# Performance work log

Measured on AMD Instinct MI355X. Metric: run time of the kernel, lower is better.

## Reference

```python
import jax, jax.numpy as jnp
import numpy as np

N, IN_F, H, D = 3072, 512, 8, 64


def setup_inputs() -> dict:
    key = jax.random.key(0)
    k1, k2, k3, k4, k5 = jax.random.split(key, 5)
    x = jax.random.normal(k1, (N, IN_F), dtype=jnp.float32)
    adj = jax.random.randint(k2, (N, N), 0, 2, dtype=jnp.int32)
    # xavier-uniform-like scales
    s_W = (6.0 / (IN_F + H * D)) ** 0.5
    s_a = (6.0 / (H + D)) ** 0.5
    W = jax.random.uniform(k3, (H * D, IN_F), dtype=jnp.float32, minval=-s_W, maxval=s_W)
    a_src = jax.random.uniform(k4, (H, D), dtype=jnp.float32, minval=-s_a, maxval=s_a)
    a_dst = jax.random.uniform(k5, (H, D), dtype=jnp.float32, minval=-s_a, maxval=s_a)
    return {"x": x, "adj": adj, "W": W, "a_src": a_src, "a_dst": a_dst}


def reference(x, adj, W, a_src, a_dst):
    n = x.shape[0]
    Hh, d = a_src.shape
    h = (x @ W.T).reshape(n, Hh, d)                      # [n, H, d]
    e_src = jnp.einsum('nhd,hd->nh', h, a_src)           # [n, H]
    e_dst = jnp.einsum('nhd,hd->nh', h, a_dst)           # [n, H]
    e = e_src[:, None, :] + e_dst[None, :, :]            # [n, n, H], e[i,j]=src_i+dst_j
    e = jax.nn.leaky_relu(e, negative_slope=0.2)
    mask = (adj + jnp.eye(n, dtype=adj.dtype)) > 0       # [n, n]
    e = jnp.where(mask[:, :, None], e, -jnp.inf)
    alpha = jax.nn.softmax(e, axis=1)                    # softmax over j (neighbors)
    # out[i,h,d] = sum_j alpha[i,j,h] * h[j,h,d]  (dropout=0 / eval mode)
    out = jnp.einsum('ijh,jhd->ihd', alpha, h)
    return out.reshape(n, Hh * d)                        # concat=True
```

## Files before the change

kernel.cpp:

```cpp
#include <hip/hip_runtime.h>
#include <hip/hip_bf16.h>

typedef __bf16 bf16x8 __attribute__((ext_vector_type(8)));
typedef _Float16 half8 __attribute__((ext_vector_type(8)));
typedef _Float16 half2v __attribute__((ext_vector_type(2)));
typedef short s16x2 __attribute__((ext_vector_type(2)));
typedef float f32x4 __attribute__((ext_vector_type(4)));
typedef float f32x16 __attribute__((ext_vector_type(16)));

#define NROW 3072
#define NF 512
#define NH 8
#define ND 64

__device__ __forceinline__ unsigned gat_enc_key(float f) {
    unsigned u = __float_as_uint(f);
    return (f < 0.f) ? ~u : (u | 0x80000000u);
}
__device__ __forceinline__ float gat_dec_key(unsigned k) {
    unsigned u = (k & 0x80000000u) ? (k ^ 0x80000000u) : ~k;
    return __uint_as_float(u);
}

__device__ __forceinline__ bf16x8 gat_ld_cvt8(const float* p) {
    float4 f0 = *reinterpret_cast<const float4*>(p);
    float4 f1 = *reinterpret_cast<const float4*>(p + 4);
    bf16x8 o = { (__bf16)f0.x, (__bf16)f0.y, (__bf16)f0.z, (__bf16)f0.w,
                 (__bf16)f1.x, (__bf16)f1.y, (__bf16)f1.z, (__bf16)f1.w };
    return o;
}

__global__ __launch_bounds__(256) void gat_bitpack(const int* __restrict__ adj,
                                                   unsigned long long* __restrict__ bits64) {
    int wave = threadIdx.x >> 6;
    int lane = threadIdx.x & 63;
    int row = blockIdx.x * 4 + wave;
    const int* p = adj + (long)row * NROW + lane;
    int v[48];
#pragma unroll
    for (int s = 0; s < 48; ++s) v[s] = p[s * 64];
    unsigned long long diag = 1ull << (row & 63);
    int dseg = row >> 6;
#pragma unroll
    for (int s = 0; s < 48; ++s) {
        unsigned long long bal = __ballot(v[s] > 0);
        if (s == dseg) bal |= diag;
        if (lane == 0) bits64[(long)row * 48 + s] = bal;
    }
}

__global__ __launch_bounds__(256) void gat_gemm(const float* __restrict__ x,
                                                const float* __restrict__ W,
                                                _Float16* __restrict__ hT,
                                                const float* __restrict__ a_src,
                                                const float* __restrict__ a_dst,
                                                float* __restrict__ e_srcT,
                                                float* __restrict__ e_dstT,
                                                unsigned* __restrict__ maxkey) {
    __shared__ __align__(16) _Float16 smem[10240];
    __shared__ float ered[2][2][2][32];

    int b = blockIdx.x;
    int i0 = (b >> 3) * 64;
    int o0 = (b & 7) * 64;
    int head = b & 7;
    int tid = threadIdx.x;
    int wave = tid >> 6;
    int lane = tid & 63;
    int half = lane >> 5;
    int l31 = lane & 31;
    int wr = wave >> 1;
    int wc = wave & 1;

    __bf16* sA = reinterpret_cast<__bf16*>(smem);
    __bf16* sB = reinterpret_cast<__bf16*>(smem) + 5120;

    int r = tid >> 2;
    int pp = tid & 3;
    const float* gA = x + (i0 + r) * NF + pp * 8;
    const float* gB = W + (o0 + r) * NF + pp * 8;
    int dslot = r * 40 + pp * 8;

    bf16x8 pA0, pB0, pA1, pB1;
    pA0 = gat_ld_cvt8(gA);
    pB0 = gat_ld_cvt8(gB);
    *reinterpret_cast<bf16x8*>(sA + dslot) = pA0;
    *reinterpret_cast<bf16x8*>(sB + dslot) = pB0;
    pA1 = gat_ld_cvt8(gA + 32);
    pB1 = gat_ld_cvt8(gB + 32);
    __syncthreads();

    f32x16 acc = {};
    int arow = (wr * 32 + l31) * 40;
    int brow = (wc * 32 + l31) * 40;

#pragma unroll
    for (int cc = 0; cc < 8; ++cc) {
        int c0 = cc * 2;
        if (c0 + 2 < 16) {
            pA0 = gat_ld_cvt8(gA + (c0 + 2) * 32);
            pB0 = gat_ld_cvt8(gB + (c0 + 2) * 32);
        }
        {
            const __bf16* pa = sA;
            const __bf16* pb = sB;
#pragma unroll
            for (int ks = 0; ks < 2; ++ks) {
                int q = (((ks << 1) | half)) << 3;
                bf16x8 a = *reinterpret_cast<const bf16x8*>(pa + arow + q);
                bf16x8 bb = *reinterpret_cast<const bf16x8*>(pb + brow + q);
                acc = __builtin_amdgcn_mfma_f32_32x32x16_bf16(a, bb, acc, 0, 0, 0);
            }
        }
        *reinterpret_cast<bf16x8*>(sA + 2560 + dslot) = pA1;
        *reinterpret_cast<bf16x8*>(sB + 2560 + dslot) = pB1;
        __syncthreads();

        int c1 = c0 + 1;
        if (c1 + 2 < 16) {
            pA1 = gat_ld_cvt8(gA + (c1 + 2) * 32);
            pB1 = gat_ld_cvt8(gB + (c1 + 2) * 32);
        }
        {
            const __bf16* pa = sA + 2560;
            const __bf16* pb = sB + 2560;
#pragma unroll
            for (int ks = 0; ks < 2; ++ks) {
                int q = (((ks << 1) | half)) << 3;
                bf16x8 a = *reinterpret_cast<const bf16x8*>(pa + arow + q);
                bf16x8 bb = *reinterpret_cast<const bf16x8*>(pb + brow + q);
                acc = __builtin_amdgcn_mfma_f32_32x32x16_bf16(a, bb, acc, 0, 0, 0);
            }
        }
        if (c1 + 1 < 16) {
            *reinterpret_cast<bf16x8*>(sA + dslot) = pA0;
            *reinterpret_cast<bf16x8*>(sB + dslot) = pB0;
        }
        __syncthreads();
    }

    _Float16* tt = smem + wave * 1280;
#pragma unroll
    for (int reg = 0; reg < 16; ++reg) {
        int rowl = (reg & 3) + 8 * (reg >> 2) + 4 * half;
        tt[rowl * 40 + l31] = (_Float16)acc[reg];
    }
    int orow = lane >> 1;
    int li = (lane & 1) * 16;
    half8 h0, h1;
#pragma unroll
    for (int t = 0; t < 8; ++t) h0[t] = tt[(li + t) * 40 + orow];
#pragma unroll
    for (int t = 0; t < 8; ++t) h1[t] = tt[(li + 8 + t) * 40 + orow];
    _Float16* op = hT + (long)(o0 + wc * 32 + orow) * NROW + i0 + wr * 32 + li;
    *reinterpret_cast<half8*>(op) = h0;
    *reinterpret_cast<half8*>(op + 8) = h1;

    half8 hv0 = *reinterpret_cast<const half8*>(tt + l31 * 40 + half * 16);
    half8 hv1 = *reinterpret_cast<const half8*>(tt + l31 * 40 + half * 16 + 8);
    const float* ap = a_src + head * ND + wc * 32 + half * 16;
    const float* dp = a_dst + head * ND + wc * 32 + half * 16;
    float4 as0 = *reinterpret_cast<const float4*>(ap);
    float4 as1 = *reinterpret_cast<const float4*>(ap + 4);
    float4 as2 = *reinterpret_cast<const float4*>(ap + 8);
    float4 as3 = *reinterpret_cast<const float4*>(ap + 12);
    float4 ad0 = *reinterpret_cast<const float4*>(dp);
    float4 ad1 = *reinterpret_cast<const float4*>(dp + 4);
    float4 ad2 = *reinterpret_cast<const float4*>(dp + 8);
    float4 ad3 = *reinterpret_cast<const float4*>(dp + 12);
    float ps = 0.f, pd = 0.f;
    ps += (float)hv0[0]*as0.x + (float)hv0[1]*as0.y + (float)hv0[2]*as0.z + (float)hv0[3]*as0.w;
    ps += (float)hv0[4]*as1.x + (float)hv0[5]*as1.y + (float)hv0[6]*as1.z + (float)hv0[7]*as1.w;
    ps += (float)hv1[0]*as2.x + (float)hv1[1]*as2.y + (float)hv1[2]*as2.z + (float)hv1[3]*as2.w;
    ps += (float)hv1[4]*as3.x + (float)hv1[5]*as3.y + (float)hv1[6]*as3.z + (float)hv1[7]*as3.w;
    pd += (float)hv0[0]*ad0.x + (float)hv0[1]*ad0.y + (float)hv0[2]*ad0.z + (float)hv0[3]*ad0.w;
    pd += (float)hv0[4]*ad1.x + (float)hv0[5]*ad1.y + (float)hv0[6]*ad1.z + (float)hv0[7]*ad1.w;
    pd += (float)hv1[0]*ad2.x + (float)hv1[1]*ad2.y + (float)hv1[2]*ad2.z + (float)hv1[3]*ad2.w;
    pd += (float)hv1[4]*ad3.x + (float)hv1[5]*ad3.y + (float)hv1[6]*ad3.z + (float)hv1[7]*ad3.w;
    ps += __shfl_xor(ps, 32, 64);
    pd += __shfl_xor(pd, 32, 64);
    if (half == 0) { ered[0][wr][wc][l31] = ps; ered[1][wr][wc][l31] = pd; }
    __syncthreads();
    if (wc == 0) {
        float pst = ered[0][wr][0][l31] + ered[0][wr][1][l31];
        float pdt = ered[1][wr][0][l31] + ered[1][wr][1][l31];
        if (half == 0) {
            e_srcT[head * NROW + i0 + wr * 32 + l31] = pst;
            e_dstT[head * NROW + i0 + wr * 32 + l31] = pdt;
        }
        float mx = pdt;
#pragma unroll
        for (int off = 1; off < 32; off <<= 1) mx = fmaxf(mx, __shfl_xor(mx, off, 64));
        if (lane == 0) atomicMax(&maxkey[head], gat_enc_key(mx));
    }
}

__global__ __launch_bounds__(256) void gat_attn(const unsigned* __restrict__ bits,
                                                const float* __restrict__ e_srcT,
                                                const float* __restrict__ e_dstT,
                                                const unsigned* __restrict__ maxkey,
                                                const _Float16* __restrict__ hT,
                                                _Float16* __restrict__ num,
                                                float* __restrict__ den) {
    constexpr int JCHUNK = NROW / 4;
    constexpr int NC = JCHUNK / 64;
    __shared__ unsigned lds_P[JCHUNK / 2];
    __shared__ unsigned lds_Q[JCHUNK / 2];
    __shared__ __align__(16) _Float16 hbuf[2][4096];
    int b = blockIdx.x;
    int head = b & 7;
    int jc = (b >> 3) & 3;
    int i0 = ((b >> 3) >> 2) * 128;
    int jbase = jc * JCHUNK;
    int tid = threadIdx.x;
    int wave = tid >> 6;
    int lane = tid & 63;
    int half = lane >> 5;
    int l31 = lane & 31;

    float Mg = gat_dec_key(maxkey[head]);
    for (int p = tid; p < JCHUNK / 2; p += 256) {
        float t0 = e_dstT[head * NROW + jbase + 2 * p] - Mg;
        float t1 = e_dstT[head * NROW + jbase + 2 * p + 1] - Mg;
        half2v P = { (_Float16)__expf(t0), (_Float16)__expf(t1) };
        half2v Q = { (_Float16)__expf(0.2f * t0), (_Float16)__expf(0.2f * t1) };
        lds_P[p] = __builtin_bit_cast(unsigned, P);
        lds_Q[p] = __builtin_bit_cast(unsigned, Q);
    }

    int irow = i0 + wave * 32 + l31;
    float u = e_srcT[head * NROW + irow] + Mg;
    float Rf = fminf(__expf(-0.8f * u), 60000.f);
    _Float16 Rh = (_Float16)Rf;
    half2v R2 = { Rh, Rh };
    const half8 ones8 = { (_Float16)1.f, (_Float16)1.f, (_Float16)1.f, (_Float16)1.f,
                          (_Float16)1.f, (_Float16)1.f, (_Float16)1.f, (_Float16)1.f };
    const unsigned* brow = bits + irow * 96 + jc * (JCHUNK / 32);

    int s0 = tid, s1 = tid + 256;
    const _Float16* gp0 = hT + (head * ND + ((s0 >> 6) & 1) * 32 + (s0 & 31)) * NROW
                             + jbase + (s0 >> 7) * 16 + ((s0 >> 5) & 1) * 8;
    const _Float16* gp1 = hT + (head * ND + ((s1 >> 6) & 1) * 32 + (s1 & 31)) * NROW
                             + jbase + (s1 >> 7) * 16 + ((s1 >> 5) & 1) * 8;
    *reinterpret_cast<half8*>(&hbuf[0][tid * 8])         = *reinterpret_cast<const half8*>(gp0);
    *reinterpret_cast<half8*>(&hbuf[0][(tid + 256) * 8]) = *reinterpret_cast<const half8*>(gp1);
    __syncthreads();

    f32x16 acc0 = {};
    f32x16 acc1 = {};
    f32x16 acc2 = {};
    uint2 wm = *reinterpret_cast<const uint2*>(brow);

    for (int k = 0; k < NC; ++k) {
        half8 st0, st1;
        uint2 wmn = wm;
        bool more = (k + 1 < NC);
        if (more) {
            st0 = *reinterpret_cast<const half8*>(gp0 + (k + 1) * 64);
            st1 = *reinterpret_cast<const half8*>(gp1 + (k + 1) * 64);
            wmn = *reinterpret_cast<const uint2*>(brow + (k + 1) * 2);
        }
        const _Float16* hb = &hbuf[k & 1][0];
#pragma unroll
        for (int js = 0; js < 4; ++js) {
            unsigned word = (js < 2) ? wm.x : wm.y;
            unsigned w8 = (word >> ((js & 1) * 16 + half * 8)) & 0xffu;
            unsigned long long S64 = ((unsigned long long)(w8 & 0x55u) << 15)
                                   | ((unsigned long long)(w8 & 0xAAu) << 30);
            uint4 Pv = *reinterpret_cast<const uint4*>(&lds_P[k * 32 + js * 8 + half * 4]);
            uint4 Qv = *reinterpret_cast<const uint4*>(&lds_Q[k * 32 + js * 8 + half * 4]);
            unsigned pr[4] = { Pv.x, Pv.y, Pv.z, Pv.w };
            unsigned qr[4] = { Qv.x, Qv.y, Qv.z, Qv.w };
            unsigned am[4];
#pragma unroll
            for (int t = 0; t < 4; ++t) {
                half2v qq = __builtin_bit_cast(half2v, qr[t]) * R2;
                half2v mx = __builtin_elementwise_max(
                                __builtin_bit_cast(half2v, pr[t]), qq);
                unsigned Wt = (unsigned)(S64 >> (2 * t));
                s16x2 mks = __builtin_bit_cast(s16x2, Wt) >> 15;
                am[t] = __builtin_bit_cast(unsigned, mx)
                      & __builtin_bit_cast(unsigned, mks);
            }
            uint4 m4 = { am[0], am[1], am[2], am[3] };
            half8 af = __builtin_bit_cast(half8, m4);
            half8 v0 = *reinterpret_cast<const half8*>(hb + (js * 128 + lane) * 8);
            half8 v1 = *reinterpret_cast<const half8*>(hb + (js * 128 + 64 + lane) * 8);
            acc0 = __builtin_amdgcn_mfma_f32_32x32x16_f16(af, v0, acc0, 0, 0, 0);
            acc1 = __builtin_amdgcn_mfma_f32_32x32x16_f16(af, v1, acc1, 0, 0, 0);
            acc2 = __builtin_amdgcn_mfma_f32_32x32x16_f16(af, ones8, acc2, 0, 0, 0);
        }
        if (more) {
            *reinterpret_cast<half8*>(&hbuf[(k + 1) & 1][tid * 8])         = st0;
            *reinterpret_cast<half8*>(&hbuf[(k + 1) & 1][(tid + 256) * 8]) = st1;
        }
        wm = wmn;
        __syncthreads();
    }

#pragma unroll
    for (int reg = 0; reg < 16; ++reg) {
        int rowl = (reg & 3) + 8 * (reg >> 2) + 4 * half;
        if (l31 == 0)
            den[(long)(jc * NROW + i0 + wave * 32 + rowl) * NH + head] = acc2[reg];
        long ob = (long)(jc * NROW + i0 + wave * 32 + rowl) * NF + head * ND + l31;
        num[ob]      = (_Float16)acc0[reg];
        num[ob + 32] = (_Float16)acc1[reg];
    }
}

__global__ __launch_bounds__(256) void gat_final(const _Float16* __restrict__ num,
                                                 const float* __restrict__ den,
                                                 float* __restrict__ out) {
    int idx = (blockIdx.x * 256 + threadIdx.x) * 8;
    int i = idx >> 9;
    int c = idx & 511;
    int head = c >> 6;
    half8 n0 = *reinterpret_cast<const half8*>(num + (long)i * NF + c);
    half8 n1 = *reinterpret_cast<const half8*>(num + (long)(NROW + i) * NF + c);
    half8 n2 = *reinterpret_cast<const half8*>(num + (long)(2 * NROW + i) * NF + c);
    half8 n3 = *reinterpret_cast<const half8*>(num + (long)(3 * NROW + i) * NF + c);
    float ds = den[i * NH + head] + den[(NROW + i) * NH + head]
             + den[(2 * NROW + i) * NH + head] + den[(3 * NROW + i) * NH + head];
    float inv = 1.0f / fmaxf(ds, 1e-30f);
    float r0 = ((float)n0[0] + (float)n1[0] + (float)n2[0] + (float)n3[0]) * inv;
    float r1 = ((float)n0[1] + (float)n1[1] + (float)n2[1] + (float)n3[1]) * inv;
    float r2 = ((float)n0[2] + (float)n1[2] + (float)n2[2] + (float)n3[2]) * inv;
    float r3 = ((float)n0[3] + (float)n1[3] + (float)n2[3] + (float)n3[3]) * inv;
    float r4 = ((float)n0[4] + (float)n1[4] + (float)n2[4] + (float)n3[4]) * inv;
    float r5 = ((float)n0[5] + (float)n1[5] + (float)n2[5] + (float)n3[5]) * inv;
    float r6 = ((float)n0[6] + (float)n1[6] + (float)n2[6] + (float)n3[6]) * inv;
    float r7 = ((float)n0[7] + (float)n1[7] + (float)n2[7] + (float)n3[7]) * inv;
    float4 o0 = { r0, r1, r2, r3 };
    float4 o1 = { r4, r5, r6, r7 };
    *reinterpret_cast<float4*>(out + idx)     = o0;
    *reinterpret_cast<float4*>(out + idx + 4) = o1;
}

extern "C" void kernel_launch(void* const* d_in, const int* in_sizes, int n_in,
                              void* d_out, int out_size, void* d_ws, size_t ws_size,
                              hipStream_t stream) {
    const float* x_raw  = (const float*)d_in[0];
    const int*   adj    = (const int*)d_in[1];
    const float* W_raw  = (const float*)d_in[2];
    const float* as_raw = (const float*)d_in[3];
    const float* ad_raw = (const float*)d_in[4];
    float* out = (float*)d_out;

    char* ws = (char*)d_ws;
    _Float16* hT     = (_Float16*)(ws);
    float*    e_srcT = (float*)(ws + 3145728);
    float*    e_dstT = (float*)(ws + 3244032);
    unsigned* maxkey = (unsigned*)(ws + 3342336);
    unsigned* bits   = (unsigned*)(ws + 3342400);
    _Float16* num    = (_Float16*)(ws + 8192064);
    float*    den    = (float*)(ws + 20774976);

    hipMemsetAsync(maxkey, 0, 64, stream);
    gat_bitpack<<<NROW / 4, 256, 0, stream>>>(adj, (unsigned long long*)bits);
    gat_gemm<<<384, 256, 0, stream>>>(x_raw, W_raw, hT, as_raw, ad_raw,
                                      e_srcT, e_dstT, maxkey);
    gat_attn<<<24 * 4 * 8, 256, 0, stream>>>(bits, e_srcT, e_dstT, maxkey, hT, num, den);
    gat_final<<<NROW * NF / 2048, 256, 0, stream>>>(num, den, out);
}
```

Baseline: 140.6 us.

## Merge bitpack into GEMM launch and double rows per attention block

The adjacency bitpack kernel is merged into the GEMM kernel as extra blocks, so the two independent stages run concurrently in one launch and one launch is removed. The attention kernel now handles 256 rows per block instead of 128, with two sets of accumulators sharing each loaded h tile and P/Q values. This halves hT global/LDS traffic per row and the grid size, but raises register pressure (six 16-float accumulators) and leaves only 384 blocks, which may reduce occupancy.

```diff
diff --git a/kernel.cpp b/kernel.cpp
--- a/kernel.cpp
+++ b/kernel.cpp
@@ -12,6 +12,8 @@
 #define NF 512
 #define NH 8
 #define ND 64
+#define BP_BLOCKS 768
+#define GEMM_BLOCKS 384
 
 __device__ __forceinline__ unsigned gat_enc_key(float f) {
     unsigned u = __float_as_uint(f);
@@ -30,43 +32,44 @@
     return o;
 }
 
-__global__ __launch_bounds__(256) void gat_bitpack(const int* __restrict__ adj,
-                                                   unsigned long long* __restrict__ bits64) {
-    int wave = threadIdx.x >> 6;
-    int lane = threadIdx.x & 63;
-    int row = blockIdx.x * 4 + wave;
-    const int* p = adj + (long)row * NROW + lane;
-    int v[48];
-#pragma unroll
-    for (int s = 0; s < 48; ++s) v[s] = p[s * 64];
-    unsigned long long diag = 1ull << (row & 63);
-    int dseg = row >> 6;
-#pragma unroll
-    for (int s = 0; s < 48; ++s) {
-        unsigned long long bal = __ballot(v[s] > 0);
-        if (s == dseg) bal |= diag;
-        if (lane == 0) bits64[(long)row * 48 + s] = bal;
-    }
-}
-
-__global__ __launch_bounds__(256) void gat_gemm(const float* __restrict__ x,
-                                                const float* __restrict__ W,
-                                                _Float16* __restrict__ hT,
-                                                const float* __restrict__ a_src,
-                                                const float* __restrict__ a_dst,
-                                                float* __restrict__ e_srcT,
-                                                float* __restrict__ e_dstT,
-                                                unsigned* __restrict__ maxkey) {
+__global__ __launch_bounds__(256) void gat_gemm_bp(const float* __restrict__ x,
+                                                   const float* __restrict__ W,
+                                                   _Float16* __restrict__ hT,
+                                                   const int* __restrict__ adj,
+                                                   unsigned long long* __restrict__ bits64,
+                                                   const float* __restrict__ a_src,
+                                                   const float* __restrict__ a_dst,
+                                                   float* __restrict__ e_srcT,
+                                                   float* __restrict__ e_dstT,
+                                                   unsigned* __restrict__ maxkey) {
     __shared__ __align__(16) _Float16 smem[10240];
     __shared__ float ered[2][2][2][32];
 
-    int b = blockIdx.x;
+    int tid = threadIdx.x;
+    int wave = tid >> 6;
+    int lane = tid & 63;
+
+    if (blockIdx.x < BP_BLOCKS) {
+        int row = blockIdx.x * 4 + wave;
+        const int* p = adj + (long)row * NROW + lane;
+        int v[48];
+#pragma unroll
+        for (int s = 0; s < 48; ++s) v[s] = p[s * 64];
+        unsigned long long diag = 1ull << (row & 63);
+        int dseg = row >> 6;
+#pragma unroll
+        for (int s = 0; s < 48; ++s) {
+            unsigned long long bal = __ballot(v[s] > 0);
+            if (s == dseg) bal |= diag;
+            if (lane == 0) bits64[(long)row * 48 + s] = bal;
+        }
+        return;
+    }
+
+    int b = blockIdx.x - BP_BLOCKS;
     int i0 = (b >> 3) * 64;
     int o0 = (b & 7) * 64;
     int head = b & 7;
-    int tid = threadIdx.x;
-    int wave = tid >> 6;
-    int lane = tid & 63;
     int half = lane >> 5;
     int l31 = lane & 31;
     int wr = wave >> 1;
@@ -210,7 +213,7 @@
     int b = blockIdx.x;
     int head = b & 7;
     int jc = (b >> 3) & 3;
-    int i0 = ((b >> 3) >> 2) * 128;
+    int i0 = (b >> 5) * 256;
     int jbase = jc * JCHUNK;
     int tid = threadIdx.x;
     int wave = tid >> 6;
@@ -228,14 +231,19 @@
         lds_Q[p] = __builtin_bit_cast(unsigned, Q);
     }
 
-    int irow = i0 + wave * 32 + l31;
-    float u = e_srcT[head * NROW + irow] + Mg;
-    float Rf = fminf(__expf(-0.8f * u), 60000.f);
-    _Float16 Rh = (_Float16)Rf;
-    half2v R2 = { Rh, Rh };
+    int irowA = i0 + wave * 32 + l31;
+    int irowB = irowA + 128;
+    float uA = e_srcT[head * NROW + irowA] + Mg;
+    float uB = e_srcT[head * NROW + irowB] + Mg;
+    float RfA = fminf(__expf(-0.8f * uA), 60000.f);
+    float RfB = fminf(__expf(-0.8f * uB), 60000.f);
+    _Float16 RhA = (_Float16)RfA, RhB = (_Float16)RfB;
+    half2v R2A = { RhA, RhA };
+    half2v R2B = { RhB, RhB };
     const half8 ones8 = { (_Float16)1.f, (_Float16)1.f, (_Float16)1.f, (_Float16)1.f,
                           (_Float16)1.f, (_Float16)1.f, (_Float16)1.f, (_Float16)1.f };
-    const unsigned* brow = bits + irow * 96 + jc * (JCHUNK / 32);
+    const unsigned* browA = bits + (long)irowA * 96 + jc * (JCHUNK / 32);
+    const unsigned* browB = bits + (long)irowB * 96 + jc * (JCHUNK / 32);
 
     int s0 = tid, s1 = tid + 256;
     const _Float16* gp0 = hT + (head * ND + ((s0 >> 6) & 1) * 32 + (s0 & 31)) * NROW
@@ -246,66 +254,84 @@
     *reinterpret_cast<half8*>(&hbuf[0][(tid + 256) * 8]) = *reinterpret_cast<const half8*>(gp1);
     __syncthreads();
 
-    f32x16 acc0 = {};
-    f32x16 acc1 = {};
-    f32x16 acc2 = {};
-    uint2 wm = *reinterpret_cast<const uint2*>(brow);
+    f32x16 acc0a = {}, acc1a = {}, acc2a = {};
+    f32x16 acc0b = {}, acc1b = {}, acc2b = {};
+    uint2 wmA = *reinterpret_cast<const uint2*>(browA);
+    uint2 wmB = *reinterpret_cast<const uint2*>(browB);
 
     for (int k = 0; k < NC; ++k) {
         half8 st0, st1;
-        uint2 wmn = wm;
+        uint2 wmnA = wmA, wmnB = wmB;
         bool more = (k + 1 < NC);
         if (more) {
             st0 = *reinterpret_cast<const half8*>(gp0 + (k + 1) * 64);
             st1 = *reinterpret_cast<const half8*>(gp1 + (k + 1) * 64);
-            wmn = *reinterpret_cast<const uint2*>(brow + (k + 1) * 2);
+            wmnA = *reinterpret_cast<const uint2*>(browA + (k + 1) * 2);
+            wmnB = *reinterpret_cast<const uint2*>(browB + (k + 1) * 2);
         }
         const _Float16* hb = &hbuf[k & 1][0];
 #pragma unroll
         for (int js = 0; js < 4; ++js) {
-            unsigned word = (js < 2) ? wm.x : wm.y;
-            unsigned w8 = (word >> ((js & 1) * 16 + half * 8)) & 0xffu;
-            unsigned long long S64 = ((unsigned long long)(w8 & 0x55u) << 15)
-                                   | ((unsigned long long)(w8 & 0xAAu) << 30);
+            int sh = (js & 1) * 16 + half * 8;
+            unsigned w8A = (((js < 2) ? wmA.x : wmA.y) >> sh) & 0xffu;
+            unsigned w8B = (((js < 2) ? wmB.x : wmB.y) >> sh) & 0xffu;
+            unsigned long long S64A = ((unsigned long long)(w8A & 0x55u) << 15)
+                                    | ((unsigned long long)(w8A & 0xAAu) << 30);
+            unsigned long long S64B = ((unsigned long long)(w8B & 0x55u) << 15)
+                                    | ((unsigned long long)(w8B & 0xAAu) << 30);
             uint4 Pv = *reinterpret_cast<const uint4*>(&lds_P[k * 32 + js * 8 + half * 4]);
             uint4 Qv = *reinterpret_cast<const uint4*>(&lds_Q[k * 32 + js * 8 + half * 4]);
             unsigned pr[4] = { Pv.x, Pv.y, Pv.z, Pv.w };
             unsigned qr[4] = { Qv.x, Qv.y, Qv.z, Qv.w };
-            unsigned am[4];
+            unsigned amA[4], amB[4];
 #pragma unroll
             for (int t = 0; t < 4; ++t) {
-                half2v qq = __builtin_bit_cast(half2v, qr[t]) * R2;
-                half2v mx = __builtin_elementwise_max(
-                                __builtin_bit_cast(half2v, pr[t]), qq);
-                unsigned Wt = (unsigned)(S64 >> (2 * t));
-                s16x2 mks = __builtin_bit_cast(s16x2, Wt) >> 15;
-                am[t] = __builtin_bit_cast(unsigned, mx)
-                      & __builtin_bit_cast(unsigned, mks);
+                half2v pv = __builtin_bit_cast(half2v, pr[t]);
+                half2v qv = __builtin_bit_cast(half2v, qr[t]);
+                half2v mxA = __builtin_elementwise_max(pv, qv * R2A);
+                half2v mxB = __builtin_elementwise_max(pv, qv * R2B);
+                s16x2 mkA = __builtin_bit_cast(s16x2, (unsigned)(S64A >> (2 * t))) >> 15;
+                s16x2 mkB = __builtin_bit_cast(s16x2, (unsigned)(S64B >> (2 * t))) >> 15;
+                amA[t] = __builtin_bit_cast(unsigned, mxA) & __builtin_bit_cast(unsigned, mkA);
+                amB[t] = __builtin_bit_cast(unsigned, mxB) & __builtin_bit_cast(unsigned, mkB);
             }
-            uint4 m4 = { am[0], am[1], am[2], am[3] };
-            half8 af = __builtin_bit_cast(half8, m4);
+            uint4 m4a = { amA[0], amA[1], amA[2], amA[3] };
+            uint4 m4b = { amB[0], amB[1], amB[2], amB[3] };
+            half8 afA = __builtin_bit_cast(half8, m4a);
+            half8 afB = __builtin_bit_cast(half8, m4b);
             half8 v0 = *reinterpret_cast<const half8*>(hb + (js * 128 + lane) * 8);
             half8 v1 = *reinterpret_cast<const half8*>(hb + (js * 128 + 64 + lane) * 8);
-            acc0 = __builtin_amdgcn_mfma_f32_32x32x16_f16(af, v0, acc0, 0, 0, 0);
-            acc1 = __builtin_amdgcn_mfma_f32_32x32x16_f16(af, v1, acc1, 0, 0, 0);
-            acc2 = __builtin_amdgcn_mfma_f32_32x32x16_f16(af, ones8, acc2, 0, 0, 0);
+            acc0a = __builtin_amdgcn_mfma_f32_32x32x16_f16(afA, v0, acc0a, 0, 0, 0);
+            acc1a = __builtin_amdgcn_mfma_f32_32x32x16_f16(afA, v1, acc1a, 0, 0, 0);
+            acc2a = __builtin_amdgcn_mfma_f32_32x32x16_f16(afA, ones8, acc2a, 0, 0, 0);
+            acc0b = __builtin_amdgcn_mfma_f32_32x32x16_f16(afB, v0, acc0b, 0, 0, 0);
+            acc1b = __builtin_amdgcn_mfma_f32_32x32x16_f16(afB, v1, acc1b, 0, 0, 0);
+            acc2b = __builtin_amdgcn_mfma_f32_32x32x16_f16(afB, ones8, acc2b, 0, 0, 0);
         }
         if (more) {
             *reinterpret_cast<half8*>(&hbuf[(k + 1) & 1][tid * 8])         = st0;
             *reinterpret_cast<half8*>(&hbuf[(k + 1) & 1][(tid + 256) * 8]) = st1;
         }
-        wm = wmn;
+        wmA = wmnA;
+        wmB = wmnB;
         __syncthreads();
     }
 
 #pragma unroll
     for (int reg = 0; reg < 16; ++reg) {
         int rowl = (reg & 3) + 8 * (reg >> 2) + 4 * half;
-        if (l31 == 0)
-            den[(long)(jc * NROW + i0 + wave * 32 + rowl) * NH + head] = acc2[reg];
-        long ob = (long)(jc * NROW + i0 + wave * 32 + rowl) * NF + head * ND + l31;
-        num[ob]      = (_Float16)acc0[reg];
-        num[ob + 32] = (_Float16)acc1[reg];
+        long rbaseA = (long)(jc * NROW + i0 + wave * 32 + rowl);
+        long rbaseB = rbaseA + 128;
+        if (l31 == 0) {
+            den[rbaseA * NH + head] = acc2a[reg];
+            den[rbaseB * NH + head] = acc2b[reg];
+        }
+        long obA = rbaseA * NF + head * ND + l31;
+        long obB = rbaseB * NF + head * ND + l31;
+        num[obA]      = (_Float16)acc0a[reg];
+        num[obA + 32] = (_Float16)acc1a[reg];
+        num[obB]      = (_Float16)acc0b[reg];
+        num[obB + 32] = (_Float16)acc1b[reg];
     }
 }
 
@@ -357,9 +383,10 @@
     float*    den    = (float*)(ws + 20774976);
 
     hipMemsetAsync(maxkey, 0, 64, stream);
-    gat_bitpack<<<NROW / 4, 256, 0, stream>>>(adj, (unsigned long long*)bits);
-    gat_gemm<<<384, 256, 0, stream>>>(x_raw, W_raw, hT, as_raw, ad_raw,
-                                      e_srcT, e_dstT, maxkey);
-    gat_attn<<<24 * 4 * 8, 256, 0, stream>>>(bits, e_srcT, e_dstT, maxkey, hT, num, den);
+    gat_gemm_bp<<<BP_BLOCKS + GEMM_BLOCKS, 256, 0, stream>>>(x_raw, W_raw, hT, adj,
+                                                             (unsigned long long*)bits,
+                                                             as_raw, ad_raw,
+                                                             e_srcT, e_dstT, maxkey);
+    gat_attn<<<12 * 4 * 8, 256, 0, stream>>>(bits, e_srcT, e_dstT, maxkey, hT, num, den);
     gat_final<<<NROW * NF / 2048, 256, 0, stream>>>(num, den, out);
 }
```

Measured after the change: 134.1 us. -4.6%, faster.
